# Kernel tuning notes

Measured on AMD Instinct MI355X. Metric: run time of the kernel, lower is better.

Reference implementation:

```python
import jax, jax.numpy as jnp
import numpy as np

N_NODES = 50000
N_EDGES = 800000
D_IN = 128
DIM = 128
N_LAYERS = 3
N_GRAPHS = 128


def setup_inputs() -> dict:
    key = jax.random.key(0)
    ks = jax.random.split(key, 10)
    x = jax.random.normal(ks[0], (N_NODES, D_IN), dtype=jnp.float32)
    edge_index = jax.random.randint(ks[1], (2, N_EDGES), 0, N_NODES, dtype=jnp.int64)
    batch = jnp.sort(jax.random.randint(ks[2], (N_NODES,), 0, N_GRAPHS, dtype=jnp.int64))
    def glorot(k, fan_in, fan_out):
        s = jnp.sqrt(6.0 / (fan_in + fan_out))
        return jax.random.uniform(k, (fan_in, fan_out), jnp.float32, -s, s)
    W0 = glorot(ks[3], D_IN, DIM)
    W1 = glorot(ks[4], DIM, DIM)
    W2 = glorot(ks[5], DIM, DIM)
    b0 = jnp.zeros((DIM,), jnp.float32)
    b1 = jnp.zeros((DIM,), jnp.float32)
    b2 = jnp.zeros((DIM,), jnp.float32)
    return {"x": x, "edge_index": edge_index, "batch": batch,
            "W0": W0, "b0": b0, "W1": W1, "b1": b1, "W2": W2, "b2": b2}


def _gcn_norm(edge_index, n_nodes):
    # add self-loops, then symmetric normalization (PyG gcn_norm)
    loops = jnp.arange(n_nodes, dtype=edge_index.dtype)
    src = jnp.concatenate([edge_index[0], loops])
    dst = jnp.concatenate([edge_index[1], loops])
    deg = jax.ops.segment_sum(jnp.ones_like(dst, dtype=jnp.float32), dst,
                              num_segments=n_nodes)
    dinv = jnp.where(deg > 0, jax.lax.rsqrt(deg), 0.0)
    norm = dinv[src] * dinv[dst]  # [E + N]
    return src, dst, norm


def _gcn_conv(x, W, b, src, dst, norm, n_nodes):
    h = x @ W                      # [N, dim]
    msgs = h[src] * norm[:, None]  # [E+N, dim] gather + edge scale
    out = jax.ops.segment_sum(msgs, dst, num_segments=n_nodes)  # scatter-add
    return out + b


def reference(x, edge_index, batch, W0, b0, W1, b1, W2, b2):
    n = x.shape[0]
    src, dst, norm = _gcn_norm(edge_index, n)
    Ws, bs = (W0, W1, W2), (b0, b1, b2)
    xs = []
    h = x
    for i in range(N_LAYERS):
        h = jax.nn.relu(_gcn_conv(h, Ws[i], bs[i], src, dst, norm, n))
        xs.append(h)
    # global mean pool per layer output
    counts = jax.ops.segment_sum(jnp.ones((n,), jnp.float32), batch,
                                 num_segments=N_GRAPHS)
    counts = jnp.maximum(counts, 1.0)[:, None]
    xpool = [jax.ops.segment_sum(h, batch, num_segments=N_GRAPHS) / counts
             for h in xs]
    return jnp.concatenate(xpool, axis=1), jnp.concatenate(xs, axis=1)
```

## Files before the change

kernel.cpp:

```cpp
#include <hip/hip_runtime.h>

#define NNODES 50000
#define NEDGES 800000
#define DIM 128
#define NGRAPHS 128
#define OUT1_STRIDE 384
#define OUT0_ELEMS (NGRAPHS * OUT1_STRIDE)
#define SCAN_CHUNK 512
#define ROWPAD 50048

typedef unsigned int uint;
typedef unsigned short ushort;
typedef short bf16x8 __attribute__((ext_vector_type(8)));
typedef float f32x4 __attribute__((ext_vector_type(4)));

union U4 { uint4 u; bf16x8 h; };

__device__ inline uint rne_bf16(float f) {
    uint b = __float_as_uint(f);
    return (b + 0x7fffu + ((b >> 16) & 1u)) >> 16;
}
__device__ inline uint pack_bf16(float lo, float hi) {
    return rne_bf16(lo) | (rne_bf16(hi) << 16);
}
__device__ inline float blo(uint u) { return __uint_as_float(u << 16); }
__device__ inline float bhi(uint u) { return __uint_as_float(u & 0xffff0000u); }

__global__ __launch_bounds__(256) void k_pre(const float* __restrict__ W0,
                                             const float* __restrict__ W1,
                                             const float* __restrict__ W2,
                                             uint* __restrict__ wz,
                                             int* __restrict__ rowcnt,
                                             uint* __restrict__ hb, int N) {
    if (blockIdx.x >= 24) {
        int i = (blockIdx.x - 24) * 256 + threadIdx.x;
        if (i < N) rowcnt[i] = 0;
        if (i < 64) hb[(size_t)N * 64 + i] = 0;
        return;
    }
    int layer = blockIdx.x >> 3;
    const float* W = (layer == 0) ? W0 : ((layer == 1) ? W1 : W2);
    int t = (blockIdx.x & 7) * 256 + threadIdx.x;
    int f = t >> 6, lane = t & 63;
    int kb = f >> 3, nt = f & 7;
    int q = lane >> 4, m = lane & 15;
    int col = nt * 16 + m;
    uint v[8];
#pragma unroll
    for (int j = 0; j < 8; ++j)
        v[j] = rne_bf16(W[(kb * 32 + q * 8 + j) * 128 + col]);
    uint4 o;
    o.x = v[0] | (v[1] << 16);
    o.y = v[2] | (v[3] << 16);
    o.z = v[4] | (v[5] << 16);
    o.w = v[6] | (v[7] << 16);
    ((uint4*)wz)[layer * 2048 + t] = o;
}

__global__ void k_count(const int* __restrict__ dst, int* __restrict__ rowcnt,
                        int* __restrict__ rank, int E) {
    int e = blockIdx.x * blockDim.x + threadIdx.x;
    if (e < E) rank[e] = atomicAdd(&rowcnt[dst[e]], 1);
}

__global__ __launch_bounds__(512) void k_sum(const int* __restrict__ cnt,
                                             int* __restrict__ bsum,
                                             float* __restrict__ dinv, int n) {
    __shared__ int red[512];
    int t = threadIdx.x;
    int i = blockIdx.x * SCAN_CHUNK + t;
    int c = (i < n) ? cnt[i] : 0;
    if (i < n) dinv[i] = rsqrtf((float)c + 1.0f);
    red[t] = c;
    __syncthreads();
    for (int off = 256; off > 0; off >>= 1) {
        if (t < off) red[t] += red[t + off];
        __syncthreads();
    }
    if (t == 0) bsum[blockIdx.x] = red[0];
}

__global__ __launch_bounds__(512) void k_writeptr(const int* __restrict__ cnt,
                                                  const int* __restrict__ bsum,
                                                  int* __restrict__ rowptr,
                                                  int n, int nb) {
    __shared__ int s[512];
    __shared__ int sb[128];
    int t = threadIdx.x;
    if (t < 128) sb[t] = (t < nb) ? bsum[t] : 0;
    __syncthreads();
    for (int off = 1; off < 128; off <<= 1) {
        int u = (t < 128 && t >= off) ? sb[t - off] : 0;
        __syncthreads();
        if (t < 128) sb[t] += u;
        __syncthreads();
    }
    int boffb = (blockIdx.x == 0) ? 0 : sb[blockIdx.x - 1];
    int i = blockIdx.x * SCAN_CHUNK + t;
    int v = (i < n) ? cnt[i] : 0;
    s[t] = v;
    __syncthreads();
    for (int off = 1; off < 512; off <<= 1) {
        int u = (t >= off) ? s[t - off] : 0;
        __syncthreads();
        s[t] += u;
        __syncthreads();
    }
    if (i < n) rowptr[i] = boffb + s[t] - v;
    if (i == n - 1) rowptr[n] = boffb + s[t];
}

__global__ void k_fill(const int* __restrict__ src, const int* __restrict__ dst,
                       const int* __restrict__ rowptr, const int* __restrict__ rank,
                       int* __restrict__ csr_src, int E) {
    int e = blockIdx.x * blockDim.x + threadIdx.x;
    if (e < E) {
        int d = dst[e];
        csr_src[rowptr[d] + rank[e]] = src[e];
    }
}

__global__ __launch_bounds__(256) void k_gemm(const float* __restrict__ A, int lda,
                                              const uint* __restrict__ Wswz,
                                              const float* __restrict__ dinv,
                                              uint* __restrict__ hb, int M) {
    __shared__ uint4 wsw[2048];
    __shared__ ushort cbuf[64 * 128];
    int tid = threadIdx.x;
#pragma unroll
    for (int i = 0; i < 8; ++i)
        wsw[i * 256 + tid] = ((const uint4*)Wswz)[i * 256 + tid];
    __syncthreads();
    int wave = tid >> 6, lane = tid & 63;
    int q = lane >> 4, m = lane & 15;
    int row0 = blockIdx.x * 64 + wave * 16;
    int arow = min(row0 + m, M - 1);
    const float* Ar = A + (size_t)arow * lda + q * 8;
    f32x4 zero = {0.0f, 0.0f, 0.0f, 0.0f};
    f32x4 acc[8];
#pragma unroll
    for (int i = 0; i < 8; ++i) acc[i] = zero;
#pragma unroll
    for (int kb = 0; kb < 4; ++kb) {
        float4 f0 = *(const float4*)(Ar + kb * 32);
        float4 f1 = *(const float4*)(Ar + kb * 32 + 4);
        U4 a;
        a.u.x = pack_bf16(f0.x, f0.y);
        a.u.y = pack_bf16(f0.z, f0.w);
        a.u.z = pack_bf16(f1.x, f1.y);
        a.u.w = pack_bf16(f1.z, f1.w);
#pragma unroll
        for (int nt = 0; nt < 8; ++nt) {
            U4 b; b.u = wsw[(kb * 8 + nt) * 64 + lane];
            acc[nt] = __builtin_amdgcn_mfma_f32_16x16x32_bf16(a.h, b.h, acc[nt], 0, 0, 0);
        }
    }
    float dv[4];
#pragma unroll
    for (int r = 0; r < 4; ++r)
        dv[r] = dinv[min(row0 + q * 4 + r, M - 1)];
    ushort* cw = cbuf + wave * 16 * 128;
#pragma unroll
    for (int nt = 0; nt < 8; ++nt)
#pragma unroll
        for (int r = 0; r < 4; ++r)
            cw[(q * 4 + r) * 128 + nt * 16 + m] = (ushort)rne_bf16(acc[nt][r] * dv[r]);
    __syncthreads();
    const uint4* cr4 = (const uint4*)cbuf;
#pragma unroll
    for (int i = 0; i < 4; ++i) {
        int c = (wave * 256) + i * 64 + lane;
        int grow = blockIdx.x * 64 + (c >> 4);
        uint4 v = cr4[c];
        if (grow < M) ((uint4*)hb)[(size_t)grow * 16 + (c & 15)] = v;
    }
}

__global__ __launch_bounds__(256) void k_agg(const uint* __restrict__ hb,
                                             const int* __restrict__ rowptr,
                                             const int* __restrict__ csr_src,
                                             const float* __restrict__ dinv,
                                             const float* __restrict__ bias,
                                             float* __restrict__ out1,
                                             int N, int layer) {
    int wave = threadIdx.x >> 6;
    int lane = threadIdx.x & 63;
    int n = blockIdx.x * 4 + wave;
    if (n >= N) return;
    int g16 = lane >> 4;
    int m16 = lane & 15;
    const uint4* hb4 = (const uint4*)hb;

    uint4 su = hb4[(size_t)n * 16 + m16];
    float sel = (g16 == 0) ? 1.0f : 0.0f;
    float a0 = sel * blo(su.x), a1 = sel * bhi(su.x);
    float a2 = sel * blo(su.y), a3 = sel * bhi(su.y);
    float a4 = sel * blo(su.z), a5 = sel * bhi(su.z);
    float a6 = sel * blo(su.w), a7 = sel * bhi(su.w);

    int beg = rowptr[n], end = rowptr[n + 1];
    for (int base = beg; base < end; base += 16) {
        int s0, s1, s2, s3;
        {
            int e0 = base + 0 + g16;
            int e1 = base + 4 + g16;
            int e2 = base + 8 + g16;
            int e3 = base + 12 + g16;
            s0 = (e0 < end) ? csr_src[e0] : N;
            s1 = (e1 < end) ? csr_src[min(e1, end - 1)] : N;
            s2 = (e2 < end) ? csr_src[min(e2, end - 1)] : N;
            s3 = (e3 < end) ? csr_src[min(e3, end - 1)] : N;
        }
        uint4 u0 = hb4[(size_t)s0 * 16 + m16];
        uint4 u1 = hb4[(size_t)s1 * 16 + m16];
        uint4 u2 = hb4[(size_t)s2 * 16 + m16];
        uint4 u3 = hb4[(size_t)s3 * 16 + m16];
        a0 += blo(u0.x); a1 += bhi(u0.x); a2 += blo(u0.y); a3 += bhi(u0.y);
        a4 += blo(u0.z); a5 += bhi(u0.z); a6 += blo(u0.w); a7 += bhi(u0.w);
        a0 += blo(u1.x); a1 += bhi(u1.x); a2 += blo(u1.y); a3 += bhi(u1.y);
        a4 += blo(u1.z); a5 += bhi(u1.z); a6 += blo(u1.w); a7 += bhi(u1.w);
        a0 += blo(u2.x); a1 += bhi(u2.x); a2 += blo(u2.y); a3 += bhi(u2.y);
        a4 += blo(u2.z); a5 += bhi(u2.z); a6 += blo(u2.w); a7 += bhi(u2.w);
        a0 += blo(u3.x); a1 += bhi(u3.x); a2 += blo(u3.y); a3 += bhi(u3.y);
        a4 += blo(u3.z); a5 += bhi(u3.z); a6 += blo(u3.w); a7 += bhi(u3.w);
    }

#pragma unroll
    for (int d = 16; d < 64; d <<= 1) {
        a0 += __shfl_xor(a0, d); a1 += __shfl_xor(a1, d);
        a2 += __shfl_xor(a2, d); a3 += __shfl_xor(a3, d);
        a4 += __shfl_xor(a4, d); a5 += __shfl_xor(a5, d);
        a6 += __shfl_xor(a6, d); a7 += __shfl_xor(a7, d);
    }

    float vx = (g16 == 0) ? a0 : (g16 == 1) ? a2 : (g16 == 2) ? a4 : a6;
    float vy = (g16 == 0) ? a1 : (g16 == 1) ? a3 : (g16 == 2) ? a5 : a7;
    float din = dinv[n];
    float2 b = ((const float2*)bias)[m16 * 4 + g16];
    float ox = fmaxf(din * vx + b.x, 0.0f);
    float oy = fmaxf(din * vy + b.y, 0.0f);
    size_t o1 = (size_t)n * OUT1_STRIDE + layer * DIM + (m16 * 8 + g16 * 2);
    *(float2*)(out1 + o1) = make_float2(ox, oy);
}

__global__ __launch_bounds__(256) void k_pool(const float* __restrict__ out1,
                                              const int* __restrict__ batch,
                                              float* __restrict__ out0, int N) {
    int g = blockIdx.x / 3;
    int chunk = blockIdx.x % 3;
    int lo = 0, hi = N;
    while (lo < hi) { int mid = (lo + hi) >> 1; if (batch[mid] < g) lo = mid + 1; else hi = mid; }
    int beg = lo;
    hi = N;
    while (lo < hi) { int mid = (lo + hi) >> 1; if (batch[mid] < g + 1) lo = mid + 1; else hi = mid; }
    int end = lo;
    int t = threadIdx.x;
    int ch = t & 127;
    int slice = t >> 7;
    const float* p = out1 + (size_t)chunk * 128 + ch;
    float acc = 0.0f;
    int i = beg + slice;
    for (; i + 6 < end; i += 8) {
        float a0 = p[(size_t)i * OUT1_STRIDE];
        float a1 = p[(size_t)(i + 2) * OUT1_STRIDE];
        float a2 = p[(size_t)(i + 4) * OUT1_STRIDE];
        float a3 = p[(size_t)(i + 6) * OUT1_STRIDE];
        acc += (a0 + a1) + (a2 + a3);
    }
    for (; i < end; i += 2) acc += p[(size_t)i * OUT1_STRIDE];
    __shared__ float red[256];
    red[t] = acc;
    __syncthreads();
    if (t < 128) {
        float tot = red[t] + red[t + 128];
        float cnt = (float)(end - beg);
        out0[(size_t)g * OUT1_STRIDE + chunk * 128 + t] = tot / fmaxf(cnt, 1.0f);
    }
}

extern "C" void kernel_launch(void* const* d_in, const int* in_sizes, int n_in,
                              void* d_out, int out_size, void* d_ws, size_t ws_size,
                              hipStream_t stream) {
    const float* x     = (const float*)d_in[0];
    const int*   ei    = (const int*)d_in[1];
    const int*   batch = (const int*)d_in[2];
    const float* W0 = (const float*)d_in[3];
    const float* b0 = (const float*)d_in[4];
    const float* W1 = (const float*)d_in[5];
    const float* b1 = (const float*)d_in[6];
    const float* W2 = (const float*)d_in[7];
    const float* b2 = (const float*)d_in[8];
    (void)n_in; (void)ws_size; (void)out_size;

    const int E = in_sizes[1] / 2;
    const int N = in_sizes[2];
    const int* src = ei;
    const int* dst = ei + E;

    char* ws = (char*)d_ws;
    uint*  hb       = (uint*)ws;  ws += (size_t)ROWPAD * 64 * 4;
    uint*  wz       = (uint*)ws;  ws += 3 * 8192 * 4;
    float* dinv     = (float*)ws; ws += 50016 * 4;
    int*   rowcnt   = (int*)ws;   ws += 50016 * 4;
    int*   rowptr   = (int*)ws;   ws += 50016 * 4;
    int*   rank     = (int*)ws;   ws += (size_t)NEDGES * 4;
    int*   csr_src  = (int*)ws;   ws += (size_t)NEDGES * 4;
    int*   bsum     = (int*)ws;   ws += 256 * 4;

    float* out0 = (float*)d_out;
    float* out1 = (float*)d_out + OUT0_ELEMS;

    const int nb  = (N + SCAN_CHUNK - 1) / SCAN_CHUNK;
    const int nbz = 24 + (N + 255) / 256;

    k_pre     <<<nbz, 256, 0, stream>>>(W0, W1, W2, wz, rowcnt, hb, N);
    k_count   <<<(E + 255) / 256, 256, 0, stream>>>(dst, rowcnt, rank, E);
    k_sum     <<<nb, 512, 0, stream>>>(rowcnt, bsum, dinv, N);
    k_writeptr<<<nb, 512, 0, stream>>>(rowcnt, bsum, rowptr, N, nb);
    k_fill    <<<(E + 255) / 256, 256, 0, stream>>>(src, dst, rowptr, rank, csr_src, E);

    const float* bs[3] = {b0, b1, b2};
    const int ngb = (N + 63) / 64;
    for (int l = 0; l < 3; ++l) {
        const float* Ain = (l == 0) ? x : (out1 + (size_t)(l - 1) * DIM);
        int lda          = (l == 0) ? DIM : OUT1_STRIDE;
        k_gemm<<<ngb, 256, 0, stream>>>(Ain, lda, wz + l * 8192, dinv, hb, N);
        k_agg <<<(N + 3) / 4, 256, 0, stream>>>(hb, rowptr, csr_src, dinv,
                                                bs[l], out1, N, l);
    }
    k_pool<<<NGRAPHS * 3, 256, 0, stream>>>(out1, batch, out0, N);
}
```

Before: 309.5 us.

## Fuse global mean pooling into aggregation via atomic adds

Result: slower. 579.1 us (+87.1%).

```diff
diff --git a/kernel.cpp b/kernel.cpp
--- a/kernel.cpp
+++ b/kernel.cpp
@@ -31,11 +31,24 @@
                                              const float* __restrict__ W2,
                                              uint* __restrict__ wz,
                                              int* __restrict__ rowcnt,
-                                             uint* __restrict__ hb, int N) {
+                                             uint* __restrict__ hb,
+                                             float* __restrict__ out0,
+                                             float* __restrict__ ginv,
+                                             const int* __restrict__ batch, int N) {
     if (blockIdx.x >= 24) {
         int i = (blockIdx.x - 24) * 256 + threadIdx.x;
         if (i < N) rowcnt[i] = 0;
         if (i < 64) hb[(size_t)N * 64 + i] = 0;
+        if (i < OUT0_ELEMS) out0[i] = 0.0f;
+        if (blockIdx.x == 24 && threadIdx.x < NGRAPHS) {
+            int g = threadIdx.x;
+            int lo = 0, hi = N;
+            while (lo < hi) { int mid = (lo + hi) >> 1; if (batch[mid] < g) lo = mid + 1; else hi = mid; }
+            int b = lo;
+            hi = N;
+            while (lo < hi) { int mid = (lo + hi) >> 1; if (batch[mid] < g + 1) lo = mid + 1; else hi = mid; }
+            ginv[g] = 1.0f / fmaxf((float)(lo - b), 1.0f);
+        }
         return;
     }
     int layer = blockIdx.x >> 3;
@@ -181,6 +194,9 @@
                                              const int* __restrict__ csr_src,
                                              const float* __restrict__ dinv,
                                              const float* __restrict__ bias,
+                                             const int* __restrict__ batch,
+                                             const float* __restrict__ ginv,
+                                             float* __restrict__ out0,
                                              float* __restrict__ out1,
                                              int N, int layer) {
     int wave = threadIdx.x >> 6;
@@ -236,46 +252,18 @@
     float vx = (g16 == 0) ? a0 : (g16 == 1) ? a2 : (g16 == 2) ? a4 : a6;
     float vy = (g16 == 0) ? a1 : (g16 == 1) ? a3 : (g16 == 2) ? a5 : a7;
     float din = dinv[n];
+    int c = m16 * 8 + g16 * 2;
     float2 b = ((const float2*)bias)[m16 * 4 + g16];
     float ox = fmaxf(din * vx + b.x, 0.0f);
     float oy = fmaxf(din * vy + b.y, 0.0f);
-    size_t o1 = (size_t)n * OUT1_STRIDE + layer * DIM + (m16 * 8 + g16 * 2);
+    size_t o1 = (size_t)n * OUT1_STRIDE + layer * DIM + c;
     *(float2*)(out1 + o1) = make_float2(ox, oy);
-}
-
-__global__ __launch_bounds__(256) void k_pool(const float* __restrict__ out1,
-                                              const int* __restrict__ batch,
-                                              float* __restrict__ out0, int N) {
-    int g = blockIdx.x / 3;
-    int chunk = blockIdx.x % 3;
-    int lo = 0, hi = N;
-    while (lo < hi) { int mid = (lo + hi) >> 1; if (batch[mid] < g) lo = mid + 1; else hi = mid; }
-    int beg = lo;
-    hi = N;
-    while (lo < hi) { int mid = (lo + hi) >> 1; if (batch[mid] < g + 1) lo = mid + 1; else hi = mid; }
-    int end = lo;
-    int t = threadIdx.x;
-    int ch = t & 127;
-    int slice = t >> 7;
-    const float* p = out1 + (size_t)chunk * 128 + ch;
-    float acc = 0.0f;
-    int i = beg + slice;
-    for (; i + 6 < end; i += 8) {
-        float a0 = p[(size_t)i * OUT1_STRIDE];
-        float a1 = p[(size_t)(i + 2) * OUT1_STRIDE];
-        float a2 = p[(size_t)(i + 4) * OUT1_STRIDE];
-        float a3 = p[(size_t)(i + 6) * OUT1_STRIDE];
-        acc += (a0 + a1) + (a2 + a3);
-    }
-    for (; i < end; i += 2) acc += p[(size_t)i * OUT1_STRIDE];
-    __shared__ float red[256];
-    red[t] = acc;
-    __syncthreads();
-    if (t < 128) {
-        float tot = red[t] + red[t + 128];
-        float cnt = (float)(end - beg);
-        out0[(size_t)g * OUT1_STRIDE + chunk * 128 + t] = tot / fmaxf(cnt, 1.0f);
-    }
+
+    int gg = batch[n];
+    float gi = ginv[gg];
+    float* o0 = out0 + (size_t)gg * OUT1_STRIDE + layer * DIM + c;
+    atomicAdd(o0, ox * gi);
+    atomicAdd(o0 + 1, oy * gi);
 }
 
 extern "C" void kernel_launch(void* const* d_in, const int* in_sizes, int n_in,
@@ -306,6 +294,7 @@
     int*   rank     = (int*)ws;   ws += (size_t)NEDGES * 4;
     int*   csr_src  = (int*)ws;   ws += (size_t)NEDGES * 4;
     int*   bsum     = (int*)ws;   ws += 256 * 4;
+    float* ginv     = (float*)ws; ws += 128 * 4;
 
     float* out0 = (float*)d_out;
     float* out1 = (float*)d_out + OUT0_ELEMS;
@@ -313,7 +302,7 @@
     const int nb  = (N + SCAN_CHUNK - 1) / SCAN_CHUNK;
     const int nbz = 24 + (N + 255) / 256;
 
-    k_pre     <<<nbz, 256, 0, stream>>>(W0, W1, W2, wz, rowcnt, hb, N);
+    k_pre     <<<nbz, 256, 0, stream>>>(W0, W1, W2, wz, rowcnt, hb, out0, ginv, batch, N);
     k_count   <<<(E + 255) / 256, 256, 0, stream>>>(dst, rowcnt, rank, E);
     k_sum     <<<nb, 512, 0, stream>>>(rowcnt, bsum, dinv, N);
     k_writeptr<<<nb, 512, 0, stream>>>(rowcnt, bsum, rowptr, N, nb);
@@ -325,8 +314,7 @@
         const float* Ain = (l == 0) ? x : (out1 + (size_t)(l - 1) * DIM);
         int lda          = (l == 0) ? DIM : OUT1_STRIDE;
         k_gemm<<<ngb, 256, 0, stream>>>(Ain, lda, wz + l * 8192, dinv, hb, N);
-        k_agg <<<(N + 3) / 4, 256, 0, stream>>>(hb, rowptr, csr_src, dinv,
-                                                bs[l], out1, N, l);
-    }
-    k_pool<<<NGRAPHS * 3, 256, 0, stream>>>(out1, batch, out0, N);
-}
+        k_agg <<<(N + 3) / 4, 256, 0, stream>>>(hb, rowptr, csr_src, dinv, bs[l],
+                                                batch, ginv, out0, out1, N, l);
+    }
+}
```
